# Performance work log

Measured on AMD Instinct MI355X. Metric: run time of the kernel, lower is better.

Reference implementation:

```python
import jax, jax.numpy as jnp
import numpy as np

B, S, D = 4, 512, 256
NEG = -1e30  # finite stand-in for -inf so fully-masked row 0 stays NaN-free


def setup_inputs() -> dict:
    key = jax.random.key(0)
    ks = jax.random.split(key, 10)
    s = 0.02
    return {
        "x": jax.random.normal(ks[0], (B, S, D), dtype=jnp.float32),
        # edge_mlp: Linear(3D -> D), ReLU, Linear(D -> 1). Stored [in, out].
        "W1": jax.random.normal(ks[1], (3 * D, D), dtype=jnp.float32) * s,
        "b1": jnp.zeros((D,), dtype=jnp.float32),
        "w2": jax.random.normal(ks[2], (D, 1), dtype=jnp.float32) * s,
        "b2": jnp.zeros((1,), dtype=jnp.float32),
        "Wv": jax.random.normal(ks[3], (D, D), dtype=jnp.float32) * s,
        "bv": jnp.zeros((D,), dtype=jnp.float32),
        "Wo": jax.random.normal(ks[4], (D, D), dtype=jnp.float32) * s,
        "bo": jnp.zeros((D,), dtype=jnp.float32),
        "gamma": jnp.ones((D,), dtype=jnp.float32),
        "beta": jnp.zeros((D,), dtype=jnp.float32),
    }


def reference(x, W1, b1, w2, b2, Wv, bv, Wo, bo, gamma, beta):
    b, seq, d = x.shape
    # edge_mlp layer1 on concat([x_i, x_j, x_i - x_j]) decomposes linearly:
    # h[b,i,j,:] = x_i @ (Wa + Wc) + x_j @ (Wb - Wc) + b1
    Wa, Wb, Wc = W1[:d], W1[d:2 * d], W1[2 * d:]
    hi = jnp.einsum('bid,dh->bih', x, Wa + Wc)          # [B,S,D]
    hj = jnp.einsum('bjd,dh->bjh', x, Wb - Wc)          # [B,S,D]
    h = jax.nn.relu(hi[:, :, None, :] + hj[:, None, :, :] + b1)  # [B,S,S,D]
    scores = jnp.einsum('bijh,h->bij', h, w2[:, 0]) + b2[0]      # [B,S,S]
    # strictly-lower-triangular causal mask (j < i)
    mask = jnp.tril(jnp.ones((seq, seq), dtype=bool), k=-1)
    scores = jnp.where(mask, scores, NEG)
    attn = jax.nn.softmax(scores, axis=-1)
    # row i=0 has no valid edges (torch yields NaN there); zero it instead
    row_valid = mask.any(axis=-1)                       # [S]
    attn = attn * row_valid[None, :, None].astype(attn.dtype)
    values = jnp.einsum('bjd,de->bje', x, Wv) + bv      # [B,S,D]
    message = jnp.einsum('bij,bjd->bid', attn, values)  # [B,S,D]
    out = jnp.einsum('bid,de->bie', message, Wo) + bo
    out = x + out
    # LayerNorm over last dim, eps=1e-5, biased variance (torch default)
    mu = jnp.mean(out, axis=-1, keepdims=True)
    var = jnp.mean(jnp.square(out - mu), axis=-1, keepdims=True)
    out = (out - mu) * jax.lax.rsqrt(var + 1e-5) * gamma + beta
    return out
```

## Files before the change

kernel.cpp:

```cpp
#include <hip/hip_runtime.h>
#include <math.h>

#define D 256
#define S 512
#define M 2048
#define CH (64 * 1024)

typedef __attribute__((ext_vector_type(8))) short bf16x8;
typedef __attribute__((ext_vector_type(4))) float f32x4;

__device__ inline ushort f2bf(float f) {
    union { float f; unsigned u; } v; v.f = f;
    unsigned r = v.u + 0x7FFFu + ((v.u >> 16) & 1u);
    return (ushort)(r >> 16);
}

__global__ __launch_bounds__(256) void qkv_pack_k(
    const float* __restrict__ x, const float* __restrict__ W1,
    const float* __restrict__ Wv, const float* __restrict__ Wo,
    const float* __restrict__ b1, const float* __restrict__ bv,
    float* __restrict__ hi, float* __restrict__ hj,
    ushort* __restrict__ vals_t, ushort* __restrict__ Wot)
{
    __shared__ union {
        ushort Bs[64][264];
        ushort lt[64][72];
    } sh;

    const int u = blockIdx.x;
    const int t = threadIdx.x;

    if (u >= 384) {
        const int unit = u - 384;
        const int a0 = (unit >> 2) * 64;
        const int b0 = (unit & 3) * 64;
        const int r = t >> 4;
        const int c = (t & 15) * 4;
#pragma unroll
        for (int p = 0; p < 4; ++p) {
            const int sr = b0 + p * 16 + r;
            float4 v = *(const float4*)(Wo + (size_t)sr * 256 + a0 + c);
            sh.lt[p * 16 + r][c + 0] = f2bf(v.x);
            sh.lt[p * 16 + r][c + 1] = f2bf(v.y);
            sh.lt[p * 16 + r][c + 2] = f2bf(v.z);
            sh.lt[p * 16 + r][c + 3] = f2bf(v.w);
        }
        __syncthreads();
#pragma unroll
        for (int p = 0; p < 4; ++p) {
            const int dr = p * 16 + r;
            ushort4 o = make_ushort4(sh.lt[c + 0][dr], sh.lt[c + 1][dr],
                                     sh.lt[c + 2][dr], sh.lt[c + 3][dr]);
            *(ushort4*)(Wot + (size_t)(a0 + dr) * 256 + b0 + c) = o;
        }
        return;
    }

    const int bn = u % 12, bm = u / 12;
    const int n0 = bn * 64, m0 = bm * 64;
    const int region = n0 >> 8, c0 = n0 & 255;

    {
        const int cl4 = (t & 15) * 4;
        const int kb = (t >> 4) * 16;
#pragma unroll
        for (int kk = 0; kk < 16; ++kk) {
            const int k = kb + kk;
            float4 v;
            if (region == 0) {
                float4 wa = *(const float4*)(W1 + (size_t)k * 256 + c0 + cl4);
                float4 wc = *(const float4*)(W1 + (size_t)(512 + k) * 256 + c0 + cl4);
                v = make_float4(wa.x + wc.x, wa.y + wc.y, wa.z + wc.z, wa.w + wc.w);
            } else if (region == 1) {
                float4 wb = *(const float4*)(W1 + (size_t)(256 + k) * 256 + c0 + cl4);
                float4 wc = *(const float4*)(W1 + (size_t)(512 + k) * 256 + c0 + cl4);
                v = make_float4(wb.x - wc.x, wb.y - wc.y, wb.z - wc.z, wb.w - wc.w);
            } else {
                v = *(const float4*)(Wv + (size_t)k * 256 + c0 + cl4);
            }
            sh.Bs[cl4 + 0][k] = f2bf(v.x);
            sh.Bs[cl4 + 1][k] = f2bf(v.y);
            sh.Bs[cl4 + 2][k] = f2bf(v.z);
            sh.Bs[cl4 + 3][k] = f2bf(v.w);
        }
    }
    __syncthreads();

    const int w = t >> 6, l = t & 63;
    const int q = l >> 4, ln = l & 15;
    const int wm = (w >> 1) * 32, wn = (w & 1) * 32;

    f32x4 acc[2][2] = {};
    for (int k0 = 0; k0 < 256; k0 += 32) {
        union { bf16x8 v; ushort s[8]; } a[2];
        bf16x8 b[2];
#pragma unroll
        for (int mt = 0; mt < 2; ++mt) {
            const float* xr = x + (size_t)(m0 + wm + mt * 16 + ln) * 256 + k0 + q * 8;
            float4 u0 = *(const float4*)xr;
            float4 u1 = *(const float4*)(xr + 4);
            a[mt].s[0] = f2bf(u0.x); a[mt].s[1] = f2bf(u0.y);
            a[mt].s[2] = f2bf(u0.z); a[mt].s[3] = f2bf(u0.w);
            a[mt].s[4] = f2bf(u1.x); a[mt].s[5] = f2bf(u1.y);
            a[mt].s[6] = f2bf(u1.z); a[mt].s[7] = f2bf(u1.w);
        }
#pragma unroll
        for (int nt = 0; nt < 2; ++nt)
            b[nt] = *(const bf16x8*)&sh.Bs[wn + nt * 16 + ln][k0 + q * 8];
#pragma unroll
        for (int mt = 0; mt < 2; ++mt)
#pragma unroll
            for (int nt = 0; nt < 2; ++nt)
                acc[mt][nt] = __builtin_amdgcn_mfma_f32_16x16x32_bf16(a[mt].v, b[nt], acc[mt][nt], 0, 0, 0);
    }

    if (region < 2) {
        float* dst = (region == 0) ? hi : hj;
#pragma unroll
        for (int nt = 0; nt < 2; ++nt) {
            const int col = c0 + wn + nt * 16 + ln;
            const float bias = (region == 0) ? b1[col] : 0.f;
#pragma unroll
            for (int mt = 0; mt < 2; ++mt)
#pragma unroll
                for (int r = 0; r < 4; ++r) {
                    const int row = m0 + wm + mt * 16 + q * 4 + r;
                    dst[(size_t)row * 256 + col] = acc[mt][nt][r] + bias;
                }
        }
    } else {
        __syncthreads();
#pragma unroll
        for (int nt = 0; nt < 2; ++nt) {
            const int cl = wn + nt * 16 + ln;
            const float bias = bv[c0 + cl];
#pragma unroll
            for (int mt = 0; mt < 2; ++mt)
#pragma unroll
                for (int r = 0; r < 4; ++r)
                    sh.lt[cl][wm + mt * 16 + q * 4 + r] = f2bf(acc[mt][nt][r] + bias);
        }
        __syncthreads();
        const int bb = m0 >> 9, jloc = m0 & 511;
#pragma unroll
        for (int p = 0; p < 2; ++p) {
            const int idx = p * 256 + t;
            const int e_l = idx & 63, jc = (idx >> 6) * 8;
            *(uint4*)(vals_t + ((size_t)(bb * 256 + c0 + e_l)) * 512 + jloc + jc) =
                *(const uint4*)&sh.lt[e_l][jc];
        }
    }
}

__global__ __launch_bounds__(256) void scores_k(
    const float* __restrict__ hi, const float* __restrict__ hj,
    const float* __restrict__ w2, float* __restrict__ sc)
{
    const int jt = blockIdx.x, it = blockIdx.y, bb = blockIdx.z;
    if (jt > 2 * it + 1) return;
    const int i0 = it * 64, j0 = jt * 32;
    const int t = threadIdx.x, w = t >> 6, l = t & 63;
    const int q = l >> 4, ln = l & 15;

    __shared__ __align__(16) float His[32][64];
    __shared__ __align__(16) float Sst[64][36];
    __shared__ float w2s[256];
    if (t < 64) *(float4*)&w2s[t * 4] = *(const float4*)(w2 + t * 4);

    const int si = t & 63, sh_ = (t >> 6) * 8;
    const float* hisrc = hi + (size_t)((bb << 9) + i0 + si) * 256 + sh_;
    const int jrow = w * 8 + q * 2;
    const float* hj0 = hj + (size_t)((bb << 9) + j0 + jrow) * 256;
    const float* hj1 = hj0 + 256;

    float acc00 = 0.f, acc01 = 0.f, acc10 = 0.f, acc11 = 0.f;
    float acc20 = 0.f, acc21 = 0.f, acc30 = 0.f, acc31 = 0.f;

    for (int hc = 0; hc < 256; hc += 32) {
        float4 a0 = *(const float4*)(hisrc + hc);
        float4 a1 = *(const float4*)(hisrc + hc + 4);
        float e0[32], e1[32];
#pragma unroll
        for (int c = 0; c < 8; ++c) {
            *(float4*)&e0[c * 4] = *(const float4*)(hj0 + hc + c * 4);
            *(float4*)&e1[c * 4] = *(const float4*)(hj1 + hc + c * 4);
        }
        __syncthreads();
        His[sh_ + 0][si] = a0.x; His[sh_ + 1][si] = a0.y;
        His[sh_ + 2][si] = a0.z; His[sh_ + 3][si] = a0.w;
        His[sh_ + 4][si] = a1.x; His[sh_ + 5][si] = a1.y;
        His[sh_ + 6][si] = a1.z; His[sh_ + 7][si] = a1.w;
        __syncthreads();
#pragma unroll
        for (int h = 0; h < 32; ++h) {
            float4 a = *(const float4*)&His[h][ln * 4];
            const float wv = w2s[hc + h];
            const float f0 = e0[h], f1 = e1[h];
            acc00 += fmaxf(a.x + f0, 0.f) * wv;
            acc01 += fmaxf(a.x + f1, 0.f) * wv;
            acc10 += fmaxf(a.y + f0, 0.f) * wv;
            acc11 += fmaxf(a.y + f1, 0.f) * wv;
            acc20 += fmaxf(a.z + f0, 0.f) * wv;
            acc21 += fmaxf(a.z + f1, 0.f) * wv;
            acc30 += fmaxf(a.w + f0, 0.f) * wv;
            acc31 += fmaxf(a.w + f1, 0.f) * wv;
        }
    }

    Sst[ln * 4 + 0][jrow] = acc00;  Sst[ln * 4 + 0][jrow + 1] = acc01;
    Sst[ln * 4 + 1][jrow] = acc10;  Sst[ln * 4 + 1][jrow + 1] = acc11;
    Sst[ln * 4 + 2][jrow] = acc20;  Sst[ln * 4 + 2][jrow + 1] = acc21;
    Sst[ln * 4 + 3][jrow] = acc30;  Sst[ln * 4 + 3][jrow + 1] = acc31;
    __syncthreads();
    const int i_l = t >> 2, jc = (t & 3) * 8;
    float* dst = sc + ((size_t)bb << 18) + (size_t)(i0 + i_l) * 512 + j0 + jc;
    *(float4*)dst       = *(const float4*)&Sst[i_l][jc];
    *(float4*)(dst + 4) = *(const float4*)&Sst[i_l][jc + 4];
}

__global__ __launch_bounds__(256) void smpvout_k(
    const float* __restrict__ sc, const ushort* __restrict__ vals_t,
    const ushort* __restrict__ Wot, const float* __restrict__ x,
    const float* __restrict__ bo, const float* __restrict__ gamma,
    const float* __restrict__ beta, float* __restrict__ out)
{
    const int u = blockIdx.x;
    const int b = u >> 5, m0 = (u & 31) * 16;
    const int t = threadIdx.x, w = t >> 6, l = t & 63;
    const int q = l >> 4, ln = l & 15;

    __shared__ __align__(16) ushort attnS[16][520];
    __shared__ __align__(16) ushort msgS[16][264];
    __shared__ float redS[16][4], redQ[16][4];

    {
        const int j0 = l * 8;
#pragma unroll
        for (int rr = 0; rr < 4; ++rr) {
            const int rl = w * 4 + rr;
            const int i = m0 + rl;
            const float* srow = sc + ((size_t)b << 18) + (size_t)i * S;
            float v[8];
            *(float4*)&v[0] = *(const float4*)(srow + j0);
            *(float4*)&v[4] = *(const float4*)(srow + j0 + 4);
            float mx = -3.0e38f;
#pragma unroll
            for (int k = 0; k < 8; ++k) {
                v[k] = (j0 + k < i) ? v[k] : -3.0e38f;
                mx = fmaxf(mx, v[k]);
            }
#pragma unroll
            for (int off = 32; off; off >>= 1) mx = fmaxf(mx, __shfl_xor(mx, off, 64));
            float e[8];
            float sum = 0.f;
#pragma unroll
            for (int k = 0; k < 8; ++k) {
                e[k] = __expf(v[k] - mx);
                sum += (j0 + k < i) ? e[k] : 0.f;
            }
#pragma unroll
            for (int off = 32; off; off >>= 1) sum += __shfl_xor(sum, off, 64);
            const float inv = (i > 0) ? (1.f / sum) : 0.f;
            ushort o[8];
#pragma unroll
            for (int k = 0; k < 8; ++k)
                o[k] = (j0 + k < i) ? f2bf(e[k] * inv) : (ushort)0;
            *(ushort4*)&attnS[rl][j0]     = make_ushort4(o[0], o[1], o[2], o[3]);
            *(ushort4*)&attnS[rl][j0 + 4] = make_ushort4(o[4], o[5], o[6], o[7]);
        }
    }
    __syncthreads();

    const ushort* V = vals_t + (size_t)b * 256 * 512;
    f32x4 acc[4] = {};
    const int kmax = (m0 + 16 + 31) & ~31;
    for (int k0 = 0; k0 < kmax; k0 += 32) {
        bf16x8 a = *(const bf16x8*)&attnS[ln][k0 + q * 8];
#pragma unroll
        for (int nt = 0; nt < 4; ++nt) {
            bf16x8 bb = *(const bf16x8*)(V + (size_t)(w * 64 + nt * 16 + ln) * 512 + k0 + q * 8);
            acc[nt] = __builtin_amdgcn_mfma_f32_16x16x32_bf16(a, bb, acc[nt], 0, 0, 0);
        }
    }
#pragma unroll
    for (int nt = 0; nt < 4; ++nt)
#pragma unroll
        for (int r = 0; r < 4; ++r)
            msgS[q * 4 + r][w * 64 + nt * 16 + ln] = f2bf(acc[nt][r]);
    __syncthreads();

    f32x4 acc2[4] = {};
    for (int k0 = 0; k0 < 256; k0 += 32) {
        bf16x8 a = *(const bf16x8*)&msgS[ln][k0 + q * 8];
#pragma unroll
        for (int nt = 0; nt < 4; ++nt) {
            bf16x8 bb = *(const bf16x8*)(Wot + (size_t)(w * 64 + nt * 16 + ln) * 256 + k0 + q * 8);
            acc2[nt] = __builtin_amdgcn_mfma_f32_16x16x32_bf16(a, bb, acc2[nt], 0, 0, 0);
        }
    }

    const int r0 = (b << 9) + m0;
    float sum[4] = {}, sq[4] = {};
#pragma unroll
    for (int nt = 0; nt < 4; ++nt) {
        const int col = w * 64 + nt * 16 + ln;
        const float bov = bo[col];
#pragma unroll
        for (int r = 0; r < 4; ++r) {
            const int row = r0 + q * 4 + r;
            float v = acc2[nt][r] + x[(size_t)row * 256 + col] + bov;
            acc2[nt][r] = v;
            sum[r] += v;
            sq[r] += v * v;
        }
    }
#pragma unroll
    for (int r = 0; r < 4; ++r) {
#pragma unroll
        for (int off = 1; off < 16; off <<= 1) {
            sum[r] += __shfl_xor(sum[r], off, 64);
            sq[r]  += __shfl_xor(sq[r],  off, 64);
        }
    }
    if (ln == 0) {
#pragma unroll
        for (int r = 0; r < 4; ++r) {
            redS[q * 4 + r][w] = sum[r];
            redQ[q * 4 + r][w] = sq[r];
        }
    }
    __syncthreads();
#pragma unroll
    for (int nt = 0; nt < 4; ++nt) {
        const int col = w * 64 + nt * 16 + ln;
        const float g = gamma[col], be = beta[col];
#pragma unroll
        for (int r = 0; r < 4; ++r) {
            const int rl = q * 4 + r;
            const float ts = redS[rl][0] + redS[rl][1] + redS[rl][2] + redS[rl][3];
            const float tq = redQ[rl][0] + redQ[rl][1] + redQ[rl][2] + redQ[rl][3];
            const float mu = ts * (1.f / 256.f);
            const float var = tq * (1.f / 256.f) - mu * mu;
            out[(size_t)(r0 + rl) * 256 + col] =
                (acc2[nt][r] - mu) * rsqrtf(var + 1e-5f) * g + be;
        }
    }
}

extern "C" void kernel_launch(void* const* d_in, const int* in_sizes, int n_in,
                              void* d_out, int out_size, void* d_ws, size_t ws_size,
                              hipStream_t stream)
{
    (void)in_sizes; (void)n_in; (void)out_size; (void)ws_size;
    const float* x     = (const float*)d_in[0];
    const float* W1    = (const float*)d_in[1];
    const float* b1    = (const float*)d_in[2];
    const float* w2    = (const float*)d_in[3];
    const float* Wv    = (const float*)d_in[5];
    const float* bv    = (const float*)d_in[6];
    const float* Wo    = (const float*)d_in[7];
    const float* bo    = (const float*)d_in[8];
    const float* gamma = (const float*)d_in[9];
    const float* beta  = (const float*)d_in[10];
    float* out = (float*)d_out;

    float* ws = (float*)d_ws;
    float*  hi     = ws;
    float*  hj     = ws + 8 * (size_t)CH;
    float*  sc     = ws + 16 * (size_t)CH;
    ushort* Wot    = (ushort*)(ws + 32 * (size_t)CH);
    ushort* vals_t = (ushort*)(ws + 33 * (size_t)CH);

    qkv_pack_k<<<dim3(400),      256, 0, stream>>>(x, W1, Wv, Wo, b1, bv, hi, hj, vals_t, Wot);
    scores_k  <<<dim3(16, 8, 4), 256, 0, stream>>>(hi, hj, w2, sc);
    smpvout_k <<<dim3(128),      256, 0, stream>>>(sc, vals_t, Wot, x, bo, gamma, beta, out);
}
```

Measured before the change: 135.1 us.

## Use packed fp16 add-relu-dot2 for edge scores and split final kernel finer

```diff
diff --git a/kernel.cpp b/kernel.cpp
--- a/kernel.cpp
+++ b/kernel.cpp
@@ -8,6 +8,7 @@
 
 typedef __attribute__((ext_vector_type(8))) short bf16x8;
 typedef __attribute__((ext_vector_type(4))) float f32x4;
+typedef _Float16 half2v __attribute__((ext_vector_type(2)));
 
 __device__ inline ushort f2bf(float f) {
     union { float f; unsigned u; } v; v.f = f;
@@ -15,11 +16,35 @@
     return (ushort)(r >> 16);
 }
 
+__device__ inline ushort f2h(float f) {
+    union { _Float16 h; ushort u; } v; v.h = (_Float16)f; return v.u;
+}
+
+__device__ inline uint pack2h(float a, float b) {
+    union { half2v h; uint u; } v; v.h[0] = (_Float16)a; v.h[1] = (_Float16)b;
+    return v.u;
+}
+
+__device__ inline uint addrelu2(uint a, uint b) {
+    union { uint u; half2v h; } x, y;
+    x.u = a; y.u = b;
+    half2v s = x.h + y.h;
+    half2v z = {};
+    s = __builtin_elementwise_max(s, z);
+    union { half2v h; uint u; } r; r.h = s; return r.u;
+}
+
+__device__ inline float fdot2u(uint a, uint b, float acc) {
+    union { uint u; half2v h; } x, y;
+    x.u = a; y.u = b;
+    return __builtin_amdgcn_fdot2(x.h, y.h, acc, false);
+}
+
 __global__ __launch_bounds__(256) void qkv_pack_k(
     const float* __restrict__ x, const float* __restrict__ W1,
     const float* __restrict__ Wv, const float* __restrict__ Wo,
     const float* __restrict__ b1, const float* __restrict__ bv,
-    float* __restrict__ hi, float* __restrict__ hj,
+    ushort* __restrict__ hi, ushort* __restrict__ hj,
     ushort* __restrict__ vals_t, ushort* __restrict__ Wot)
 {
     __shared__ union {
@@ -115,7 +140,7 @@
     }
 
     if (region < 2) {
-        float* dst = (region == 0) ? hi : hj;
+        ushort* dst = (region == 0) ? hi : hj;
 #pragma unroll
         for (int nt = 0; nt < 2; ++nt) {
             const int col = c0 + wn + nt * 16 + ln;
@@ -125,7 +150,7 @@
 #pragma unroll
                 for (int r = 0; r < 4; ++r) {
                     const int row = m0 + wm + mt * 16 + q * 4 + r;
-                    dst[(size_t)row * 256 + col] = acc[mt][nt][r] + bias;
+                    dst[(size_t)row * 256 + col] = f2h(acc[mt][nt][r] + bias);
                 }
         }
     } else {
@@ -153,7 +178,7 @@
 }
 
 __global__ __launch_bounds__(256) void scores_k(
-    const float* __restrict__ hi, const float* __restrict__ hj,
+    const ushort* __restrict__ hi, const ushort* __restrict__ hj,
     const float* __restrict__ w2, float* __restrict__ sc)
 {
     const int jt = blockIdx.x, it = blockIdx.y, bb = blockIdx.z;
@@ -162,48 +187,52 @@
     const int t = threadIdx.x, w = t >> 6, l = t & 63;
     const int q = l >> 4, ln = l & 15;
 
-    __shared__ __align__(16) float His[32][64];
+    __shared__ __align__(16) uint His2u[16][64];
     __shared__ __align__(16) float Sst[64][36];
-    __shared__ float w2s[256];
-    if (t < 64) *(float4*)&w2s[t * 4] = *(const float4*)(w2 + t * 4);
+    __shared__ uint w2u[128];
+    if (t < 64) {
+        float4 wv = *(const float4*)(w2 + t * 4);
+        w2u[t * 2 + 0] = pack2h(wv.x, wv.y);
+        w2u[t * 2 + 1] = pack2h(wv.z, wv.w);
+    }
 
     const int si = t & 63, sh_ = (t >> 6) * 8;
-    const float* hisrc = hi + (size_t)((bb << 9) + i0 + si) * 256 + sh_;
+    const ushort* hisrc = hi + (size_t)((bb << 9) + i0 + si) * 256 + sh_;
     const int jrow = w * 8 + q * 2;
-    const float* hj0 = hj + (size_t)((bb << 9) + j0 + jrow) * 256;
-    const float* hj1 = hj0 + 256;
+    const ushort* hj0 = hj + (size_t)((bb << 9) + j0 + jrow) * 256;
+    const ushort* hj1 = hj0 + 256;
 
     float acc00 = 0.f, acc01 = 0.f, acc10 = 0.f, acc11 = 0.f;
     float acc20 = 0.f, acc21 = 0.f, acc30 = 0.f, acc31 = 0.f;
 
     for (int hc = 0; hc < 256; hc += 32) {
-        float4 a0 = *(const float4*)(hisrc + hc);
-        float4 a1 = *(const float4*)(hisrc + hc + 4);
-        float e0[32], e1[32];
-#pragma unroll
-        for (int c = 0; c < 8; ++c) {
-            *(float4*)&e0[c * 4] = *(const float4*)(hj0 + hc + c * 4);
-            *(float4*)&e1[c * 4] = *(const float4*)(hj1 + hc + c * 4);
+        uint4 a = *(const uint4*)(hisrc + hc);
+        uint e0u[16], e1u[16];
+#pragma unroll
+        for (int c = 0; c < 4; ++c) {
+            *(uint4*)&e0u[c * 4] = *(const uint4*)(hj0 + hc + c * 8);
+            *(uint4*)&e1u[c * 4] = *(const uint4*)(hj1 + hc + c * 8);
         }
         __syncthreads();
-        His[sh_ + 0][si] = a0.x; His[sh_ + 1][si] = a0.y;
-        His[sh_ + 2][si] = a0.z; His[sh_ + 3][si] = a0.w;
-        His[sh_ + 4][si] = a1.x; His[sh_ + 5][si] = a1.y;
-        His[sh_ + 6][si] = a1.z; His[sh_ + 7][si] = a1.w;
+        const int hp0 = sh_ >> 1;
+        His2u[hp0 + 0][si] = a.x;
+        His2u[hp0 + 1][si] = a.y;
+        His2u[hp0 + 2][si] = a.z;
+        His2u[hp0 + 3][si] = a.w;
         __syncthreads();
 #pragma unroll
-        for (int h = 0; h < 32; ++h) {
-            float4 a = *(const float4*)&His[h][ln * 4];
-            const float wv = w2s[hc + h];
-            const float f0 = e0[h], f1 = e1[h];
-            acc00 += fmaxf(a.x + f0, 0.f) * wv;
-            acc01 += fmaxf(a.x + f1, 0.f) * wv;
-            acc10 += fmaxf(a.y + f0, 0.f) * wv;
-            acc11 += fmaxf(a.y + f1, 0.f) * wv;
-            acc20 += fmaxf(a.z + f0, 0.f) * wv;
-            acc21 += fmaxf(a.z + f1, 0.f) * wv;
-            acc30 += fmaxf(a.w + f0, 0.f) * wv;
-            acc31 += fmaxf(a.w + f1, 0.f) * wv;
+        for (int hp = 0; hp < 16; ++hp) {
+            uint4 av = *(const uint4*)&His2u[hp][ln * 4];
+            const uint wv = w2u[(hc >> 1) + hp];
+            const uint f0 = e0u[hp], f1 = e1u[hp];
+            acc00 = fdot2u(addrelu2(av.x, f0), wv, acc00);
+            acc01 = fdot2u(addrelu2(av.x, f1), wv, acc01);
+            acc10 = fdot2u(addrelu2(av.y, f0), wv, acc10);
+            acc11 = fdot2u(addrelu2(av.y, f1), wv, acc11);
+            acc20 = fdot2u(addrelu2(av.z, f0), wv, acc20);
+            acc21 = fdot2u(addrelu2(av.z, f1), wv, acc21);
+            acc30 = fdot2u(addrelu2(av.w, f0), wv, acc30);
+            acc31 = fdot2u(addrelu2(av.w, f1), wv, acc31);
         }
     }
 
@@ -218,100 +247,100 @@
     *(float4*)(dst + 4) = *(const float4*)&Sst[i_l][jc + 4];
 }
 
-__global__ __launch_bounds__(256) void smpvout_k(
+__global__ __launch_bounds__(512) void smpvout_k(
     const float* __restrict__ sc, const ushort* __restrict__ vals_t,
     const ushort* __restrict__ Wot, const float* __restrict__ x,
     const float* __restrict__ bo, const float* __restrict__ gamma,
     const float* __restrict__ beta, float* __restrict__ out)
 {
     const int u = blockIdx.x;
-    const int b = u >> 5, m0 = (u & 31) * 16;
+    const int b = u >> 6, m0 = (u & 63) * 8;
     const int t = threadIdx.x, w = t >> 6, l = t & 63;
     const int q = l >> 4, ln = l & 15;
 
     __shared__ __align__(16) ushort attnS[16][520];
     __shared__ __align__(16) ushort msgS[16][264];
-    __shared__ float redS[16][4], redQ[16][4];
+    __shared__ float redS[8][8], redQ[8][8];
+
+    *(uint4*)&attnS[8 + (t >> 6)][(t & 63) * 8] = make_uint4(0, 0, 0, 0);
 
     {
+        const int i = m0 + w;
+        const float* srow = sc + ((size_t)b << 18) + (size_t)i * S;
         const int j0 = l * 8;
-#pragma unroll
-        for (int rr = 0; rr < 4; ++rr) {
-            const int rl = w * 4 + rr;
-            const int i = m0 + rl;
-            const float* srow = sc + ((size_t)b << 18) + (size_t)i * S;
-            float v[8];
-            *(float4*)&v[0] = *(const float4*)(srow + j0);
-            *(float4*)&v[4] = *(const float4*)(srow + j0 + 4);
-            float mx = -3.0e38f;
-#pragma unroll
-            for (int k = 0; k < 8; ++k) {
-                v[k] = (j0 + k < i) ? v[k] : -3.0e38f;
-                mx = fmaxf(mx, v[k]);
-            }
-#pragma unroll
-            for (int off = 32; off; off >>= 1) mx = fmaxf(mx, __shfl_xor(mx, off, 64));
-            float e[8];
-            float sum = 0.f;
-#pragma unroll
-            for (int k = 0; k < 8; ++k) {
-                e[k] = __expf(v[k] - mx);
-                sum += (j0 + k < i) ? e[k] : 0.f;
-            }
-#pragma unroll
-            for (int off = 32; off; off >>= 1) sum += __shfl_xor(sum, off, 64);
-            const float inv = (i > 0) ? (1.f / sum) : 0.f;
-            ushort o[8];
-#pragma unroll
-            for (int k = 0; k < 8; ++k)
-                o[k] = (j0 + k < i) ? f2bf(e[k] * inv) : (ushort)0;
-            *(ushort4*)&attnS[rl][j0]     = make_ushort4(o[0], o[1], o[2], o[3]);
-            *(ushort4*)&attnS[rl][j0 + 4] = make_ushort4(o[4], o[5], o[6], o[7]);
-        }
+        float v[8];
+        *(float4*)&v[0] = *(const float4*)(srow + j0);
+        *(float4*)&v[4] = *(const float4*)(srow + j0 + 4);
+        float mx = -3.0e38f;
+#pragma unroll
+        for (int k = 0; k < 8; ++k) {
+            v[k] = (j0 + k < i) ? v[k] : -3.0e38f;
+            mx = fmaxf(mx, v[k]);
+        }
+#pragma unroll
+        for (int off = 32; off; off >>= 1) mx = fmaxf(mx, __shfl_xor(mx, off, 64));
+        float e[8];
+        float sum = 0.f;
+#pragma unroll
+        for (int k = 0; k < 8; ++k) {
+            e[k] = __expf(v[k] - mx);
+            sum += (j0 + k < i) ? e[k] : 0.f;
+        }
+#pragma unroll
+        for (int off = 32; off; off >>= 1) sum += __shfl_xor(sum, off, 64);
+        const float inv = (i > 0) ? (1.f / sum) : 0.f;
+        ushort o[8];
+#pragma unroll
+        for (int k = 0; k < 8; ++k)
+            o[k] = (j0 + k < i) ? f2bf(e[k] * inv) : (ushort)0;
+        *(ushort4*)&attnS[w][j0]     = make_ushort4(o[0], o[1], o[2], o[3]);
+        *(ushort4*)&attnS[w][j0 + 4] = make_ushort4(o[4], o[5], o[6], o[7]);
     }
     __syncthreads();
 
     const ushort* V = vals_t + (size_t)b * 256 * 512;
-    f32x4 acc[4] = {};
-    const int kmax = (m0 + 16 + 31) & ~31;
+    f32x4 acc[2] = {};
+    const int kmax = (m0 + 8 + 31) & ~31;
     for (int k0 = 0; k0 < kmax; k0 += 32) {
         bf16x8 a = *(const bf16x8*)&attnS[ln][k0 + q * 8];
 #pragma unroll
-        for (int nt = 0; nt < 4; ++nt) {
-            bf16x8 bb = *(const bf16x8*)(V + (size_t)(w * 64 + nt * 16 + ln) * 512 + k0 + q * 8);
+        for (int nt = 0; nt < 2; ++nt) {
+            bf16x8 bb = *(const bf16x8*)(V + (size_t)(w * 32 + nt * 16 + ln) * 512 + k0 + q * 8);
             acc[nt] = __builtin_amdgcn_mfma_f32_16x16x32_bf16(a, bb, acc[nt], 0, 0, 0);
         }
     }
 #pragma unroll
-    for (int nt = 0; nt < 4; ++nt)
+    for (int nt = 0; nt < 2; ++nt)
 #pragma unroll
         for (int r = 0; r < 4; ++r)
-            msgS[q * 4 + r][w * 64 + nt * 16 + ln] = f2bf(acc[nt][r]);
+            msgS[q * 4 + r][w * 32 + nt * 16 + ln] = f2bf(acc[nt][r]);
     __syncthreads();
 
-    f32x4 acc2[4] = {};
+    f32x4 acc2[2] = {};
     for (int k0 = 0; k0 < 256; k0 += 32) {
         bf16x8 a = *(const bf16x8*)&msgS[ln][k0 + q * 8];
 #pragma unroll
-        for (int nt = 0; nt < 4; ++nt) {
-            bf16x8 bb = *(const bf16x8*)(Wot + (size_t)(w * 64 + nt * 16 + ln) * 256 + k0 + q * 8);
+        for (int nt = 0; nt < 2; ++nt) {
+            bf16x8 bb = *(const bf16x8*)(Wot + (size_t)(w * 32 + nt * 16 + ln) * 256 + k0 + q * 8);
             acc2[nt] = __builtin_amdgcn_mfma_f32_16x16x32_bf16(a, bb, acc2[nt], 0, 0, 0);
         }
     }
 
     const int r0 = (b << 9) + m0;
     float sum[4] = {}, sq[4] = {};
-#pragma unroll
-    for (int nt = 0; nt < 4; ++nt) {
-        const int col = w * 64 + nt * 16 + ln;
-        const float bov = bo[col];
-#pragma unroll
-        for (int r = 0; r < 4; ++r) {
-            const int row = r0 + q * 4 + r;
-            float v = acc2[nt][r] + x[(size_t)row * 256 + col] + bov;
-            acc2[nt][r] = v;
-            sum[r] += v;
-            sq[r] += v * v;
+    if (q < 2) {
+#pragma unroll
+        for (int nt = 0; nt < 2; ++nt) {
+            const int col = w * 32 + nt * 16 + ln;
+            const float bov = bo[col];
+#pragma unroll
+            for (int r = 0; r < 4; ++r) {
+                const int row = r0 + q * 4 + r;
+                float v = acc2[nt][r] + x[(size_t)row * 256 + col] + bov;
+                acc2[nt][r] = v;
+                sum[r] += v;
+                sq[r] += v * v;
+            }
         }
     }
 #pragma unroll
@@ -322,7 +351,7 @@
             sq[r]  += __shfl_xor(sq[r],  off, 64);
         }
     }
-    if (ln == 0) {
+    if (ln == 0 && q < 2) {
 #pragma unroll
         for (int r = 0; r < 4; ++r) {
             redS[q * 4 + r][w] = sum[r];
@@ -330,19 +359,22 @@
         }
     }
     __syncthreads();
-#pragma unroll
-    for (int nt = 0; nt < 4; ++nt) {
-        const int col = w * 64 + nt * 16 + ln;
-        const float g = gamma[col], be = beta[col];
-#pragma unroll
-        for (int r = 0; r < 4; ++r) {
-            const int rl = q * 4 + r;
-            const float ts = redS[rl][0] + redS[rl][1] + redS[rl][2] + redS[rl][3];
-            const float tq = redQ[rl][0] + redQ[rl][1] + redQ[rl][2] + redQ[rl][3];
-            const float mu = ts * (1.f / 256.f);
-            const float var = tq * (1.f / 256.f) - mu * mu;
-            out[(size_t)(r0 + rl) * 256 + col] =
-                (acc2[nt][r] - mu) * rsqrtf(var + 1e-5f) * g + be;
+    if (q < 2) {
+#pragma unroll
+        for (int nt = 0; nt < 2; ++nt) {
+            const int col = w * 32 + nt * 16 + ln;
+            const float g = gamma[col], be = beta[col];
+#pragma unroll
+            for (int r = 0; r < 4; ++r) {
+                const int rl = q * 4 + r;
+                float ts = 0.f, tq = 0.f;
+#pragma unroll
+                for (int k = 0; k < 8; ++k) { ts += redS[rl][k]; tq += redQ[rl][k]; }
+                const float mu = ts * (1.f / 256.f);
+                const float var = tq * (1.f / 256.f) - mu * mu;
+                out[(size_t)(r0 + rl) * 256 + col] =
+                    (acc2[nt][r] - mu) * rsqrtf(var + 1e-5f) * g + be;
+            }
         }
     }
 }
@@ -365,13 +397,13 @@
     float* out = (float*)d_out;
 
     float* ws = (float*)d_ws;
-    float*  hi     = ws;
-    float*  hj     = ws + 8 * (size_t)CH;
+    ushort* hi     = (ushort*)ws;
+    ushort* hj     = (ushort*)(ws + 8 * (size_t)CH);
     float*  sc     = ws + 16 * (size_t)CH;
     ushort* Wot    = (ushort*)(ws + 32 * (size_t)CH);
     ushort* vals_t = (ushort*)(ws + 33 * (size_t)CH);
 
     qkv_pack_k<<<dim3(400),      256, 0, stream>>>(x, W1, Wv, Wo, b1, bv, hi, hj, vals_t, Wot);
     scores_k  <<<dim3(16, 8, 4), 256, 0, stream>>>(hi, hj, w2, sc);
-    smpvout_k <<<dim3(128),      256, 0, stream>>>(sc, vals_t, Wot, x, bo, gamma, beta, out);
-}
+    smpvout_k <<<dim3(256),      512, 0, stream>>>(sc, vals_t, Wot, x, bo, gamma, beta, out);
+}
```

After: 126.4 us. 1.07x faster.
